# Performance work log

Hardware: AMD Instinct MI355X
Metric: run time of the kernel (lower is better)

## Reference

```python
import jax, jax.numpy as jnp
import numpy as np

N = 50000
E = 1600000
D_IN = 768
NHID = 256
NCLASS = 2


def _spmm(rows, cols, vals, dense):
    # out[i] = sum_{e: rows[e]==i} vals[e] * dense[cols[e]]
    return jax.ops.segment_sum(vals[:, None] * dense[cols], rows, num_segments=N)


def _att_fusion(x1, x2, x3, w):
    # a: [N,3] -> abs -> softmax over the 3 branches
    a = jnp.abs(jnp.concatenate([x1, x2, x3], axis=-1) @ w)
    a = jax.nn.softmax(a, axis=-1)  # [N,3]
    x = jnp.stack([x1, x2, x3], axis=-1)  # [N,H,3]
    return jnp.sum(x * a[:, None, :], axis=-1)  # [N,H]


def setup_inputs() -> dict:
    key = jax.random.key(0)
    ks = jax.random.split(key, 24)

    def u(k, shape, fan):
        s = 1.0 / np.sqrt(fan)
        return jax.random.uniform(k, shape, jnp.float32, -s, s)

    inp = {
        "x": jax.random.normal(ks[0], (N, D_IN), jnp.float32),
        "adj_rows": jax.random.randint(ks[1], (E,), 0, N, jnp.int32),
        "adj_cols": jax.random.randint(ks[2], (E,), 0, N, jnp.int32),
        "adj_vals": jax.random.uniform(ks[3], (E,), jnp.float32),
        "s_rows": jax.random.randint(ks[4], (E,), 0, N, jnp.int32),
        "s_cols": jax.random.randint(ks[5], (E,), 0, N, jnp.int32),
        "s_vals": jax.random.uniform(ks[6], (E,), jnp.float32),
        "W1r1": u(ks[7], (D_IN, NHID), NHID),
        "b1r1": u(ks[8], (NHID,), NHID),
        "W1r2": u(ks[9], (D_IN, NHID), NHID),
        "b1r2": u(ks[10], (NHID,), NHID),
        "mlp1_W": u(ks[11], (D_IN, NHID), D_IN),
        "mlp1_b": u(ks[12], (NHID,), D_IN),
        "af1_w": u(ks[13], (3 * NHID, 3), 3 * NHID),
        "W2r1": u(ks[14], (NHID, NCLASS), NCLASS),
        "b2r1": u(ks[15], (NCLASS,), NCLASS),
        "W2r2": u(ks[16], (NHID, NCLASS), NCLASS),
        "b2r2": u(ks[17], (NCLASS,), NCLASS),
        "mlp2_W": u(ks[18], (NHID, NCLASS), NHID),
        "mlp2_b": u(ks[19], (NCLASS,), NHID),
    }
    return inp


def reference(x, adj_rows, adj_cols, adj_vals, s_rows, s_cols, s_vals,
              W1r1, b1r1, W1r2, b1r2, mlp1_W, mlp1_b, af1_w,
              W2r1, b2r1, W2r2, b2r2, mlp2_W, mlp2_b):
    # dropout in eval mode -> identity
    # layer 1: two sparse GCN branches + tanh MLP branch, attention fused
    x_r1 = _spmm(adj_rows, adj_cols, adj_vals, x @ W1r1) + b1r1
    x_r2 = _spmm(s_rows, s_cols, s_vals, x @ W1r2) + b1r2
    x_1 = jnp.tanh(x @ mlp1_W + mlp1_b)
    x1 = _att_fusion(x_r1, x_r2, x_1, af1_w)  # [N, NHID]

    # layer 2: summed branches
    y_r1 = _spmm(adj_rows, adj_cols, adj_vals, x1 @ W2r1) + b2r1
    y_r2 = _spmm(s_rows, s_cols, s_vals, x1 @ W2r2) + b2r2
    y_1 = jnp.tanh(x1 @ mlp2_W + mlp2_b)
    return y_r2 + y_r1 + y_1  # [N, NCLASS]
```

## Files before the change

kernel.cpp:

```cpp
#include <hip/hip_runtime.h>
#include <hip/hip_bf16.h>

#define NN 50000
#define EE 1600000
#define DIN 768
#define NH 256

typedef unsigned short u16;
typedef unsigned int u32;

typedef __attribute__((ext_vector_type(8))) short short8;
typedef __attribute__((ext_vector_type(4))) float f32x4;

__device__ __forceinline__ float bf2f(u16 u) {
  union { u32 i; float f; } x; x.i = ((u32)u) << 16; return x.f;
}
__device__ __forceinline__ u16 f2bf(float f) {
  union { float f; u32 u; } x; x.f = f;
  u32 r = x.u + 0x7fff + ((x.u >> 16) & 1);
  return (u16)(r >> 16);
}

__global__ __launch_bounds__(256) void prep_kernel(
    const float* __restrict__ X, u16* __restrict__ Xb,
    const int* __restrict__ rA, const int* __restrict__ rB,
    int* __restrict__ cntA, int* __restrict__ cntB,
    const float* __restrict__ Wa, const float* __restrict__ Wb,
    const float* __restrict__ Wc, u16* __restrict__ Wt) {
  int b = blockIdx.x;
  if (b < 37500) {
    size_t idx = (size_t)b * 256 + threadIdx.x;
    float4 v = reinterpret_cast<const float4*>(X)[idx];
    ushort4 o;
    o.x = f2bf(v.x); o.y = f2bf(v.y); o.z = f2bf(v.z); o.w = f2bf(v.w);
    reinterpret_cast<ushort4*>(Xb)[idx] = o;
  } else if (b < 50000) {
    int e = (b - 37500) * 256 + threadIdx.x;
    if (e < EE) atomicAdd(&cntA[rA[e]], 1);
    else        atomicAdd(&cntB[rB[e - EE]], 1);
  } else {
    int idx = (b - 50000) * 256 + threadIdx.x;
    int n = idx / DIN, k = idx - n * DIN;
    const float* W = (n < 256) ? Wa : (n < 512) ? Wb : Wc;
    Wt[idx] = f2bf(W[(size_t)k * NH + (n & 255)]);
  }
}

__global__ __launch_bounds__(256) void scan1(int* __restrict__ cntA, int* __restrict__ rsA,
                                             int* __restrict__ cntB, int* __restrict__ rsB,
                                             int* __restrict__ bsum) {
  int* cnt = (blockIdx.y == 0) ? cntA : cntB;
  int* rs  = (blockIdx.y == 0) ? rsA  : rsB;
  int* bs  = bsum + blockIdx.y * 98;
  __shared__ int wsum[4];
  int t = threadIdx.x, lane = t & 63, wid = t >> 6;
  int i0 = blockIdx.x * 512 + 2 * t;
  int v0 = (i0 < NN) ? cnt[i0] : 0;
  int v1 = (i0 + 1 < NN) ? cnt[i0 + 1] : 0;
  int s = v0 + v1;
  int sc = s;
#pragma unroll
  for (int off = 1; off < 64; off <<= 1) {
    int tv = __shfl_up(sc, off, 64);
    if (lane >= off) sc += tv;
  }
  if (lane == 63) wsum[wid] = sc;
  __syncthreads();
  int woff = 0;
  for (int w = 0; w < wid; ++w) woff += wsum[w];
  int excl = woff + sc - s;
  if (i0 < NN)     { cnt[i0] = excl;          rs[i0 + 1] = excl + v0; }
  if (i0 + 1 < NN) { cnt[i0 + 1] = excl + v0; rs[i0 + 2] = excl + v0 + v1; }
  if (t == 255) bs[blockIdx.x] = woff + sc;
  if (blockIdx.x == 0 && t == 0) rs[0] = 0;
}

__global__ __launch_bounds__(128) void scan2(int* __restrict__ bsum) {
  int* bs = bsum + blockIdx.y * 98;
  __shared__ int tmp[128];
  int t = threadIdx.x;
  int orig = (t < 98) ? bs[t] : 0;
  tmp[t] = orig;
  __syncthreads();
  for (int off = 1; off < 128; off <<= 1) {
    int v = (t >= off) ? tmp[t - off] : 0;
    __syncthreads();
    tmp[t] += v;
    __syncthreads();
  }
  if (t < 98) bs[t] = tmp[t] - orig;
}

__global__ __launch_bounds__(512) void scan3(int* __restrict__ cntA, int* __restrict__ rsA,
                                             int* __restrict__ cntB, int* __restrict__ rsB,
                                             const int* __restrict__ bsum) {
  int* cnt = (blockIdx.y == 0) ? cntA : cntB;
  int* rs  = (blockIdx.y == 0) ? rsA  : rsB;
  int off = bsum[blockIdx.y * 98 + blockIdx.x];
  int i = blockIdx.x * 512 + threadIdx.x;
  if (i < NN) { cnt[i] += off; rs[i + 1] += off; }
}

#define TM 128
#define TN 128
#define TK 32
#define GEMM_BLKS 2346
#define TOT_BLKS (GEMM_BLKS + 12500)

__device__ __forceinline__ void gload16(const u16* g, u16* lds) {
  __builtin_amdgcn_global_load_lds((const __attribute__((address_space(1))) unsigned int*)g,
                                   (__attribute__((address_space(3))) unsigned int*)lds, 16, 0, 0);
}

__global__ __launch_bounds__(256) void gemm_scatter(
    const u16* __restrict__ Xb, const u16* __restrict__ Wt, const float* __restrict__ mlp1_b,
    u16* __restrict__ H1, u16* __restrict__ H2, u16* __restrict__ T,
    const int* __restrict__ rA, const int* __restrict__ cA, const float* __restrict__ vA,
    const int* __restrict__ rB, const int* __restrict__ cB, const float* __restrict__ vB,
    int* __restrict__ curA, u32* __restrict__ edgeA,
    int* __restrict__ curB, u32* __restrict__ edgeB) {
  __shared__ u16 As[TM * TK];
  __shared__ u16 Bs[TN * TK];

  const int b = blockIdx.x;
  const int lo = (b * GEMM_BLKS) / TOT_BLKS;
  const int hi = ((b + 1) * GEMM_BLKS) / TOT_BLKS;

  if (hi > lo) {
    const int gid = lo;
    const int tid = threadIdx.x;
    const int lane = tid & 63;
    const int w = tid >> 6;
    const int n0 = (gid % 6) * TN;
    const int m0 = (gid / 6) * TM;
    const int wm = w >> 1, wn = w & 1;

    f32x4 acc[4][4] = {};

    const int r_l = lane >> 2;
    const int kcp = lane & 3;
    const int r16 = lane & 15;
    const int kcl = lane >> 4;

    for (int k0 = 0; k0 < DIN; k0 += TK) {
#pragma unroll
      for (int q = 0; q < 2; ++q) {
        int row = w * 32 + q * 16 + r_l;
        int kc = kcp ^ ((row >> 1) & 3);
        int gr = m0 + row; if (gr >= NN) gr = NN - 1;
        gload16(Xb + (size_t)gr * DIN + k0 + kc * 8, &As[(w * 32 + q * 16) * TK]);
        gload16(Wt + (size_t)(n0 + row) * DIN + k0 + kc * 8, &Bs[(w * 32 + q * 16) * TK]);
      }
      __syncthreads();

      short8 aF[4], bF[4];
#pragma unroll
      for (int i = 0; i < 4; ++i) {
        int m = wm * 64 + i * 16 + r16;
        aF[i] = *reinterpret_cast<const short8*>(&As[m * TK + (kcl ^ ((m >> 1) & 3)) * 8]);
        int n = wn * 64 + i * 16 + r16;
        bF[i] = *reinterpret_cast<const short8*>(&Bs[n * TK + (kcl ^ ((n >> 1) & 3)) * 8]);
      }
#pragma unroll
      for (int i = 0; i < 4; ++i)
#pragma unroll
        for (int j = 0; j < 4; ++j)
          acc[i][j] = __builtin_amdgcn_mfma_f32_16x16x32_bf16(aF[i], bF[j], acc[i][j], 0, 0, 0);
      __syncthreads();
    }

    const int bsel = n0 >> 8;
    u16* O = (bsel == 0) ? H1 : (bsel == 1) ? H2 : T;
    const int act = (bsel == 2);
    const int cb = n0 & 255;
    const int rq = lane >> 4;
#pragma unroll
    for (int i = 0; i < 4; ++i) {
#pragma unroll
      for (int rr = 0; rr < 4; ++rr) {
        int grow = m0 + wm * 64 + i * 16 + rq * 4 + rr;
        if (grow >= NN) continue;
#pragma unroll
        for (int j = 0; j < 4; ++j) {
          int c = cb + wn * 64 + j * 16 + r16;
          float v = acc[i][j][rr];
          if (act) v = tanhf(v + mlp1_b[c]);
          O[(size_t)grow * NH + c] = f2bf(v);
        }
      }
    }
  } else {
    const int sid = b - lo;
    int e = sid * 256 + threadIdx.x;
    if (e < EE) {
      int r = rA[e];
      int p = atomicAdd(&curA[r], 1);
      edgeA[p] = (u32)(u16)cA[e] | ((u32)f2bf(vA[e]) << 16);
    } else {
      e -= EE;
      int r = rB[e];
      int p = atomicAdd(&curB[r], 1);
      edgeB[p] = (u32)(u16)cB[e] | ((u32)f2bf(vB[e]) << 16);
    }
  }
}

__global__ __launch_bounds__(256) void spmm_fuse(
    const int* __restrict__ rsA, const u32* __restrict__ edgeA,
    const u16* __restrict__ H1, const float* __restrict__ b1,
    const int* __restrict__ rsB, const u32* __restrict__ edgeB,
    const u16* __restrict__ H2, const float* __restrict__ b2,
    const u16* __restrict__ T, const float* __restrict__ afw,
    const float* __restrict__ W2r1, const float* __restrict__ W2r2,
    const float* __restrict__ mlpW, const float* __restrict__ mlpb,
    float* __restrict__ Z1, float* __restrict__ Z2, float* __restrict__ Y1) {
  __shared__ float w[DIN * 3];
  __shared__ float w1[NH * 2], w2[NH * 2], wmm[NH * 2];
  int tid = threadIdx.x;
  for (int i = tid; i < DIN * 3; i += 256) w[i] = afw[i];
  for (int i = tid; i < NH * 2; i += 256) { w1[i] = W2r1[i]; w2[i] = W2r2[i]; wmm[i] = mlpW[i]; }
  __syncthreads();

  int lane = tid & 63, wv = tid >> 6;
  int n = blockIdx.x * 4 + wv;
  int h0 = (lane & 31) * 8;
  int eg = lane >> 5;

  float ac1[8] = {}, ac2[8] = {};
  {
    int s = rsA[n], e = rsA[n + 1];
    int i = s + eg;
    for (; i + 6 < e; i += 8) {
      u32 e0 = edgeA[i], e1 = edgeA[i + 2], e2 = edgeA[i + 4], e3 = edgeA[i + 6];
      short8 v0 = *reinterpret_cast<const short8*>(H1 + (size_t)(e0 & 0xFFFF) * NH + h0);
      short8 v1 = *reinterpret_cast<const short8*>(H1 + (size_t)(e1 & 0xFFFF) * NH + h0);
      short8 v2 = *reinterpret_cast<const short8*>(H1 + (size_t)(e2 & 0xFFFF) * NH + h0);
      short8 v3 = *reinterpret_cast<const short8*>(H1 + (size_t)(e3 & 0xFFFF) * NH + h0);
      float f0 = bf2f((u16)(e0 >> 16)), f1 = bf2f((u16)(e1 >> 16));
      float f2 = bf2f((u16)(e2 >> 16)), f3 = bf2f((u16)(e3 >> 16));
#pragma unroll
      for (int j = 0; j < 8; ++j)
        ac1[j] += f0 * bf2f((u16)v0[j]) + f1 * bf2f((u16)v1[j])
                + f2 * bf2f((u16)v2[j]) + f3 * bf2f((u16)v3[j]);
    }
    for (; i < e; i += 2) {
      u32 e0 = edgeA[i];
      short8 v0 = *reinterpret_cast<const short8*>(H1 + (size_t)(e0 & 0xFFFF) * NH + h0);
      float f0 = bf2f((u16)(e0 >> 16));
#pragma unroll
      for (int j = 0; j < 8; ++j) ac1[j] += f0 * bf2f((u16)v0[j]);
    }
  }
  {
    int s = rsB[n], e = rsB[n + 1];
    int i = s + eg;
    for (; i + 6 < e; i += 8) {
      u32 e0 = edgeB[i], e1 = edgeB[i + 2], e2 = edgeB[i + 4], e3 = edgeB[i + 6];
      short8 v0 = *reinterpret_cast<const short8*>(H2 + (size_t)(e0 & 0xFFFF) * NH + h0);
      short8 v1 = *reinterpret_cast<const short8*>(H2 + (size_t)(e1 & 0xFFFF) * NH + h0);
      short8 v2 = *reinterpret_cast<const short8*>(H2 + (size_t)(e2 & 0xFFFF) * NH + h0);
      short8 v3 = *reinterpret_cast<const short8*>(H2 + (size_t)(e3 & 0xFFFF) * NH + h0);
      float f0 = bf2f((u16)(e0 >> 16)), f1 = bf2f((u16)(e1 >> 16));
      float f2 = bf2f((u16)(e2 >> 16)), f3 = bf2f((u16)(e3 >> 16));
#pragma unroll
      for (int j = 0; j < 8; ++j)
        ac2[j] += f0 * bf2f((u16)v0[j]) + f1 * bf2f((u16)v1[j])
                + f2 * bf2f((u16)v2[j]) + f3 * bf2f((u16)v3[j]);
    }
    for (; i < e; i += 2) {
      u32 e0 = edgeB[i];
      short8 v0 = *reinterpret_cast<const short8*>(H2 + (size_t)(e0 & 0xFFFF) * NH + h0);
      float f0 = bf2f((u16)(e0 >> 16));
#pragma unroll
      for (int j = 0; j < 8; ++j) ac2[j] += f0 * bf2f((u16)v0[j]);
    }
  }
#pragma unroll
  for (int j = 0; j < 8; ++j) {
    ac1[j] += __shfl_xor(ac1[j], 32, 64);
    ac2[j] += __shfl_xor(ac2[j], 32, 64);
  }

  float r1[8], r2[8], t8[8];
  {
    float4 bA0 = *reinterpret_cast<const float4*>(b1 + h0);
    float4 bA1 = *reinterpret_cast<const float4*>(b1 + h0 + 4);
    float4 bB0 = *reinterpret_cast<const float4*>(b2 + h0);
    float4 bB1 = *reinterpret_cast<const float4*>(b2 + h0 + 4);
    float bbA[8] = {bA0.x, bA0.y, bA0.z, bA0.w, bA1.x, bA1.y, bA1.z, bA1.w};
    float bbB[8] = {bB0.x, bB0.y, bB0.z, bB0.w, bB1.x, bB1.y, bB1.z, bB1.w};
    short8 tv = *reinterpret_cast<const short8*>(T + (size_t)n * NH + h0);
#pragma unroll
    for (int j = 0; j < 8; ++j) {
      r1[j] = ac1[j] + bbA[j];
      r2[j] = ac2[j] + bbB[j];
      t8[j] = bf2f((u16)tv[j]);
    }
  }

  float l0 = 0.f, l1 = 0.f, l2 = 0.f;
#pragma unroll
  for (int k = 0; k < 8; ++k) {
    int h = h0 + k;
    l0 += r1[k] * w[h * 3 + 0] + r2[k] * w[(NH + h) * 3 + 0] + t8[k] * w[(2 * NH + h) * 3 + 0];
    l1 += r1[k] * w[h * 3 + 1] + r2[k] * w[(NH + h) * 3 + 1] + t8[k] * w[(2 * NH + h) * 3 + 1];
    l2 += r1[k] * w[h * 3 + 2] + r2[k] * w[(NH + h) * 3 + 2] + t8[k] * w[(2 * NH + h) * 3 + 2];
  }
#pragma unroll
  for (int off = 16; off > 0; off >>= 1) {
    l0 += __shfl_xor(l0, off, 64);
    l1 += __shfl_xor(l1, off, 64);
    l2 += __shfl_xor(l2, off, 64);
  }
  l0 = fabsf(l0); l1 = fabsf(l1); l2 = fabsf(l2);
  float mx = fmaxf(l0, fmaxf(l1, l2));
  float e0 = expf(l0 - mx), e1 = expf(l1 - mx), e2 = expf(l2 - mx);
  float inv = 1.f / (e0 + e1 + e2);
  float s0 = e0 * inv, s1 = e1 * inv, s2 = e2 * inv;

  float p10 = 0.f, p11 = 0.f, p20 = 0.f, p21 = 0.f, p30 = 0.f, p31 = 0.f;
#pragma unroll
  for (int k = 0; k < 8; ++k) {
    int h = h0 + k;
    float xv = s0 * r1[k] + s1 * r2[k] + s2 * t8[k];
    p10 += xv * w1[h * 2 + 0]; p11 += xv * w1[h * 2 + 1];
    p20 += xv * w2[h * 2 + 0]; p21 += xv * w2[h * 2 + 1];
    p30 += xv * wmm[h * 2 + 0]; p31 += xv * wmm[h * 2 + 1];
  }
#pragma unroll
  for (int off = 16; off > 0; off >>= 1) {
    p10 += __shfl_xor(p10, off, 64); p11 += __shfl_xor(p11, off, 64);
    p20 += __shfl_xor(p20, off, 64); p21 += __shfl_xor(p21, off, 64);
    p30 += __shfl_xor(p30, off, 64); p31 += __shfl_xor(p31, off, 64);
  }
  if (lane == 0) {
    Z1[n * 2 + 0] = p10; Z1[n * 2 + 1] = p11;
    Z2[n * 2 + 0] = p20; Z2[n * 2 + 1] = p21;
    Y1[n * 2 + 0] = tanhf(p30 + mlpb[0]);
    Y1[n * 2 + 1] = tanhf(p31 + mlpb[1]);
  }
}

__global__ __launch_bounds__(256) void spmm2_final(
    const int* __restrict__ rsA, const u32* __restrict__ edgeA,
    const int* __restrict__ rsB, const u32* __restrict__ edgeB,
    const float* __restrict__ Z1, const float* __restrict__ Z2, const float* __restrict__ Y1,
    const float* __restrict__ b2r1, const float* __restrict__ b2r2,
    float* __restrict__ out) {
  int tid = threadIdx.x;
  int lane = tid & 63, wave = tid >> 6;
  int n = blockIdx.x * 4 + wave;
  float a0 = 0.f, a1 = 0.f;
  {
    int s = rsA[n], e = rsA[n + 1];
    for (int i = s + lane; i < e; i += 64) {
      u32 ed = edgeA[i];
      float v = bf2f((u16)(ed >> 16));
      float2 z = *reinterpret_cast<const float2*>(Z1 + (ed & 0xFFFF) * 2);
      a0 += v * z.x; a1 += v * z.y;
    }
  }
  float c0 = 0.f, c1 = 0.f;
  {
    int s = rsB[n], e = rsB[n + 1];
    for (int i = s + lane; i < e; i += 64) {
      u32 ed = edgeB[i];
      float v = bf2f((u16)(ed >> 16));
      float2 z = *reinterpret_cast<const float2*>(Z2 + (ed & 0xFFFF) * 2);
      c0 += v * z.x; c1 += v * z.y;
    }
  }
#pragma unroll
  for (int off = 32; off > 0; off >>= 1) {
    a0 += __shfl_down(a0, off, 64); a1 += __shfl_down(a1, off, 64);
    c0 += __shfl_down(c0, off, 64); c1 += __shfl_down(c1, off, 64);
  }
  if (lane == 0) {
    out[n * 2 + 0] = (a0 + b2r1[0]) + (c0 + b2r2[0]) + Y1[n * 2 + 0];
    out[n * 2 + 1] = (a1 + b2r1[1]) + (c1 + b2r2[1]) + Y1[n * 2 + 1];
  }
}

extern "C" void kernel_launch(void* const* d_in, const int* in_sizes, int n_in,
                              void* d_out, int out_size, void* d_ws, size_t ws_size,
                              hipStream_t stream) {
  const float* x        = (const float*)d_in[0];
  const int*   adj_rows = (const int*)d_in[1];
  const int*   adj_cols = (const int*)d_in[2];
  const float* adj_vals = (const float*)d_in[3];
  const int*   s_rows   = (const int*)d_in[4];
  const int*   s_cols   = (const int*)d_in[5];
  const float* s_vals   = (const float*)d_in[6];
  const float* W1r1     = (const float*)d_in[7];
  const float* b1r1     = (const float*)d_in[8];
  const float* W1r2     = (const float*)d_in[9];
  const float* b1r2     = (const float*)d_in[10];
  const float* mlp1_W   = (const float*)d_in[11];
  const float* mlp1_b   = (const float*)d_in[12];
  const float* af1_w    = (const float*)d_in[13];
  const float* W2r1     = (const float*)d_in[14];
  const float* b2r1     = (const float*)d_in[15];
  const float* W2r2     = (const float*)d_in[16];
  const float* b2r2     = (const float*)d_in[17];
  const float* mlp2_W   = (const float*)d_in[18];
  const float* mlp2_b   = (const float*)d_in[19];
  float* out = (float*)d_out;

  char* p = (char*)d_ws;
  auto alloc = [&](size_t b) { char* r = p; p += (b + 255) & ~(size_t)255; return r; };

  char* xb_region = alloc((size_t)NN * DIN * 2);
  u16* Xb = (u16*)xb_region;
  float* Z1 = (float*)xb_region;
  float* Z2 = (float*)(xb_region + (size_t)NN * 2 * 4);
  float* Y1 = (float*)(xb_region + (size_t)NN * 4 * 4);

  u16* H1 = (u16*)alloc((size_t)NN * NH * 2);
  u16* H2 = (u16*)alloc((size_t)NN * NH * 2);
  u16* T  = (u16*)alloc((size_t)NN * NH * 2);
  u16* Wt = (u16*)alloc((size_t)DIN * DIN * 2);
  int* rsA   = (int*)alloc((size_t)(NN + 1) * 4);
  int* curA  = (int*)alloc((size_t)NN * 4);
  u32* edgeA = (u32*)alloc((size_t)EE * 4);
  int* rsB   = (int*)alloc((size_t)(NN + 1) * 4);
  int* curB  = (int*)alloc((size_t)NN * 4);
  u32* edgeB = (u32*)alloc((size_t)EE * 4);
  int* bsum  = (int*)alloc(2 * 98 * 4);

  hipMemsetAsync(curA, 0, (size_t)NN * 4, stream);
  hipMemsetAsync(curB, 0, (size_t)NN * 4, stream);
  prep_kernel<<<52304, 256, 0, stream>>>(x, Xb, adj_rows, s_rows, curA, curB,
                                         W1r1, W1r2, mlp1_W, Wt);

  dim3 gsc(98, 2);
  scan1<<<gsc, 256, 0, stream>>>(curA, rsA, curB, rsB, bsum);
  scan2<<<dim3(1, 2), 128, 0, stream>>>(bsum);
  scan3<<<gsc, 512, 0, stream>>>(curA, rsA, curB, rsB, bsum);

  gemm_scatter<<<TOT_BLKS, 256, 0, stream>>>(Xb, Wt, mlp1_b, H1, H2, T,
                                             adj_rows, adj_cols, adj_vals,
                                             s_rows, s_cols, s_vals,
                                             curA, edgeA, curB, edgeB);

  spmm_fuse<<<NN / 4, 256, 0, stream>>>(rsA, edgeA, H1, b1r1,
                                        rsB, edgeB, H2, b1r2,
                                        T, af1_w, W2r1, W2r2, mlp2_W, mlp2_b,
                                        Z1, Z2, Y1);

  spmm2_final<<<NN / 4, 256, 0, stream>>>(rsA, edgeA, rsB, edgeB,
                                          Z1, Z2, Y1, b2r1, b2r2, out);
}
```

Baseline: 905.6 us.

## Fold scan2 into scan3, batch scatter edges, deepen SpMM unrolling, split final SpMM by half-wave

Drops the separate scan2 launch: each scan3 block now loads the 98 block sums into shared memory and adds up its own prefix. The scatter blocks each handle 4 edges per thread, with row loads, packing and atomics issued in separate batches to expose more memory parallelism. The layer-1 SpMM gains a 16-edge unrolled loop that issues 8 gathers before accumulating. The final SpMM has each half-wave process one adjacency instead of running both sequentially across the full wave. Together these aim to cut launch overhead and raise memory-level parallelism, at the cost of more registers and a changed block balance in the fused GEMM/scatter grid.

```diff
diff --git a/kernel.cpp b/kernel.cpp
--- a/kernel.cpp
+++ b/kernel.cpp
@@ -75,28 +75,16 @@
   if (blockIdx.x == 0 && t == 0) rs[0] = 0;
 }
 
-__global__ __launch_bounds__(128) void scan2(int* __restrict__ bsum) {
-  int* bs = bsum + blockIdx.y * 98;
-  __shared__ int tmp[128];
-  int t = threadIdx.x;
-  int orig = (t < 98) ? bs[t] : 0;
-  tmp[t] = orig;
-  __syncthreads();
-  for (int off = 1; off < 128; off <<= 1) {
-    int v = (t >= off) ? tmp[t - off] : 0;
-    __syncthreads();
-    tmp[t] += v;
-    __syncthreads();
-  }
-  if (t < 98) bs[t] = tmp[t] - orig;
-}
-
 __global__ __launch_bounds__(512) void scan3(int* __restrict__ cntA, int* __restrict__ rsA,
                                              int* __restrict__ cntB, int* __restrict__ rsB,
                                              const int* __restrict__ bsum) {
   int* cnt = (blockIdx.y == 0) ? cntA : cntB;
   int* rs  = (blockIdx.y == 0) ? rsA  : rsB;
-  int off = bsum[blockIdx.y * 98 + blockIdx.x];
+  __shared__ int bs[98];
+  if (threadIdx.x < 98) bs[threadIdx.x] = bsum[blockIdx.y * 98 + threadIdx.x];
+  __syncthreads();
+  int off = 0;
+  for (int k = 0; k < blockIdx.x; ++k) off += bs[k];
   int i = blockIdx.x * 512 + threadIdx.x;
   if (i < NN) { cnt[i] += off; rs[i + 1] += off; }
 }
@@ -105,7 +93,8 @@
 #define TN 128
 #define TK 32
 #define GEMM_BLKS 2346
-#define TOT_BLKS (GEMM_BLKS + 12500)
+#define SCAT_BLKS 3125
+#define TOT_BLKS (GEMM_BLKS + SCAT_BLKS)
 
 __device__ __forceinline__ void gload16(const u16* g, u16* lds) {
   __builtin_amdgcn_global_load_lds((const __attribute__((address_space(1))) unsigned int*)g,
@@ -191,16 +180,24 @@
     }
   } else {
     const int sid = b - lo;
-    int e = sid * 256 + threadIdx.x;
-    if (e < EE) {
-      int r = rA[e];
-      int p = atomicAdd(&curA[r], 1);
-      edgeA[p] = (u32)(u16)cA[e] | ((u32)f2bf(vA[e]) << 16);
-    } else {
-      e -= EE;
-      int r = rB[e];
-      int p = atomicAdd(&curB[r], 1);
-      edgeB[p] = (u32)(u16)cB[e] | ((u32)f2bf(vB[e]) << 16);
+    const int base = sid * 1024 + threadIdx.x;
+    int rws[4]; u32 pks[4];
+#pragma unroll
+    for (int q = 0; q < 4; ++q) {
+      int e = base + q * 256;
+      rws[q] = (e < EE) ? rA[e] : rB[e - EE];
+    }
+#pragma unroll
+    for (int q = 0; q < 4; ++q) {
+      int e = base + q * 256;
+      if (e < EE) pks[q] = (u32)(u16)cA[e] | ((u32)f2bf(vA[e]) << 16);
+      else        pks[q] = (u32)(u16)cB[e - EE] | ((u32)f2bf(vB[e - EE]) << 16);
+    }
+#pragma unroll
+    for (int q = 0; q < 4; ++q) {
+      int e = base + q * 256;
+      if (e < EE) { int p = atomicAdd(&curA[rws[q]], 1); edgeA[p] = pks[q]; }
+      else        { int p = atomicAdd(&curB[rws[q]], 1); edgeB[p] = pks[q]; }
     }
   }
 }
@@ -230,18 +227,35 @@
   {
     int s = rsA[n], e = rsA[n + 1];
     int i = s + eg;
+    for (; i + 14 < e; i += 16) {
+      u32 ew[8];
+#pragma unroll
+      for (int q = 0; q < 8; ++q) ew[q] = edgeA[i + 2 * q];
+      short8 hv[8];
+#pragma unroll
+      for (int q = 0; q < 8; ++q)
+        hv[q] = *reinterpret_cast<const short8*>(H1 + (size_t)(ew[q] & 0xFFFF) * NH + h0);
+#pragma unroll
+      for (int q = 0; q < 8; ++q) {
+        float f = bf2f((u16)(ew[q] >> 16));
+#pragma unroll
+        for (int j = 0; j < 8; ++j) ac1[j] += f * bf2f((u16)hv[q][j]);
+      }
+    }
     for (; i + 6 < e; i += 8) {
-      u32 e0 = edgeA[i], e1 = edgeA[i + 2], e2 = edgeA[i + 4], e3 = edgeA[i + 6];
-      short8 v0 = *reinterpret_cast<const short8*>(H1 + (size_t)(e0 & 0xFFFF) * NH + h0);
-      short8 v1 = *reinterpret_cast<const short8*>(H1 + (size_t)(e1 & 0xFFFF) * NH + h0);
-      short8 v2 = *reinterpret_cast<const short8*>(H1 + (size_t)(e2 & 0xFFFF) * NH + h0);
-      short8 v3 = *reinterpret_cast<const short8*>(H1 + (size_t)(e3 & 0xFFFF) * NH + h0);
-      float f0 = bf2f((u16)(e0 >> 16)), f1 = bf2f((u16)(e1 >> 16));
-      float f2 = bf2f((u16)(e2 >> 16)), f3 = bf2f((u16)(e3 >> 16));
-#pragma unroll
-      for (int j = 0; j < 8; ++j)
-        ac1[j] += f0 * bf2f((u16)v0[j]) + f1 * bf2f((u16)v1[j])
-                + f2 * bf2f((u16)v2[j]) + f3 * bf2f((u16)v3[j]);
+      u32 ew[4];
+#pragma unroll
+      for (int q = 0; q < 4; ++q) ew[q] = edgeA[i + 2 * q];
+      short8 hv[4];
+#pragma unroll
+      for (int q = 0; q < 4; ++q)
+        hv[q] = *reinterpret_cast<const short8*>(H1 + (size_t)(ew[q] & 0xFFFF) * NH + h0);
+#pragma unroll
+      for (int q = 0; q < 4; ++q) {
+        float f = bf2f((u16)(ew[q] >> 16));
+#pragma unroll
+        for (int j = 0; j < 8; ++j) ac1[j] += f * bf2f((u16)hv[q][j]);
+      }
     }
     for (; i < e; i += 2) {
       u32 e0 = edgeA[i];
@@ -254,18 +268,35 @@
   {
     int s = rsB[n], e = rsB[n + 1];
     int i = s + eg;
+    for (; i + 14 < e; i += 16) {
+      u32 ew[8];
+#pragma unroll
+      for (int q = 0; q < 8; ++q) ew[q] = edgeB[i + 2 * q];
+      short8 hv[8];
+#pragma unroll
+      for (int q = 0; q < 8; ++q)
+        hv[q] = *reinterpret_cast<const short8*>(H2 + (size_t)(ew[q] & 0xFFFF) * NH + h0);
+#pragma unroll
+      for (int q = 0; q < 8; ++q) {
+        float f = bf2f((u16)(ew[q] >> 16));
+#pragma unroll
+        for (int j = 0; j < 8; ++j) ac2[j] += f * bf2f((u16)hv[q][j]);
+      }
+    }
     for (; i + 6 < e; i += 8) {
-      u32 e0 = edgeB[i], e1 = edgeB[i + 2], e2 = edgeB[i + 4], e3 = edgeB[i + 6];
-      short8 v0 = *reinterpret_cast<const short8*>(H2 + (size_t)(e0 & 0xFFFF) * NH + h0);
-      short8 v1 = *reinterpret_cast<const short8*>(H2 + (size_t)(e1 & 0xFFFF) * NH + h0);
-      short8 v2 = *reinterpret_cast<const short8*>(H2 + (size_t)(e2 & 0xFFFF) * NH + h0);
-      short8 v3 = *reinterpret_cast<const short8*>(H2 + (size_t)(e3 & 0xFFFF) * NH + h0);
-      float f0 = bf2f((u16)(e0 >> 16)), f1 = bf2f((u16)(e1 >> 16));
-      float f2 = bf2f((u16)(e2 >> 16)), f3 = bf2f((u16)(e3 >> 16));
-#pragma unroll
-      for (int j = 0; j < 8; ++j)
-        ac2[j] += f0 * bf2f((u16)v0[j]) + f1 * bf2f((u16)v1[j])
-                + f2 * bf2f((u16)v2[j]) + f3 * bf2f((u16)v3[j]);
+      u32 ew[4];
+#pragma unroll
+      for (int q = 0; q < 4; ++q) ew[q] = edgeB[i + 2 * q];
+      short8 hv[4];
+#pragma unroll
+      for (int q = 0; q < 4; ++q)
+        hv[q] = *reinterpret_cast<const short8*>(H2 + (size_t)(ew[q] & 0xFFFF) * NH + h0);
+#pragma unroll
+      for (int q = 0; q < 4; ++q) {
+        float f = bf2f((u16)(ew[q] >> 16));
+#pragma unroll
+        for (int j = 0; j < 8; ++j) ac2[j] += f * bf2f((u16)hv[q][j]);
+      }
     }
     for (; i < e; i += 2) {
       u32 e0 = edgeB[i];
@@ -350,34 +381,37 @@
   int tid = threadIdx.x;
   int lane = tid & 63, wave = tid >> 6;
   int n = blockIdx.x * 4 + wave;
+  int half = lane >> 5, l32 = lane & 31;
+  const int* rs = half ? rsB : rsA;
+  const u32* edge = half ? edgeB : edgeA;
+  const float* Z = half ? Z2 : Z1;
   float a0 = 0.f, a1 = 0.f;
-  {
-    int s = rsA[n], e = rsA[n + 1];
-    for (int i = s + lane; i < e; i += 64) {
-      u32 ed = edgeA[i];
-      float v = bf2f((u16)(ed >> 16));
-      float2 z = *reinterpret_cast<const float2*>(Z1 + (ed & 0xFFFF) * 2);
-      a0 += v * z.x; a1 += v * z.y;
-    }
-  }
-  float c0 = 0.f, c1 = 0.f;
-  {
-    int s = rsB[n], e = rsB[n + 1];
-    for (int i = s + lane; i < e; i += 64) {
-      u32 ed = edgeB[i];
-      float v = bf2f((u16)(ed >> 16));
-      float2 z = *reinterpret_cast<const float2*>(Z2 + (ed & 0xFFFF) * 2);
-      c0 += v * z.x; c1 += v * z.y;
-    }
-  }
-#pragma unroll
-  for (int off = 32; off > 0; off >>= 1) {
-    a0 += __shfl_down(a0, off, 64); a1 += __shfl_down(a1, off, 64);
-    c0 += __shfl_down(c0, off, 64); c1 += __shfl_down(c1, off, 64);
-  }
+  int s = rs[n], e = rs[n + 1];
+  int i = s + l32;
+  for (; i + 32 < e; i += 64) {
+    u32 e0 = edge[i], e1 = edge[i + 32];
+    float v0 = bf2f((u16)(e0 >> 16)), v1 = bf2f((u16)(e1 >> 16));
+    float2 z0 = *reinterpret_cast<const float2*>(Z + (e0 & 0xFFFF) * 2);
+    float2 z1 = *reinterpret_cast<const float2*>(Z + (e1 & 0xFFFF) * 2);
+    a0 += v0 * z0.x + v1 * z1.x;
+    a1 += v0 * z0.y + v1 * z1.y;
+  }
+  if (i < e) {
+    u32 e0 = edge[i];
+    float v0 = bf2f((u16)(e0 >> 16));
+    float2 z0 = *reinterpret_cast<const float2*>(Z + (e0 & 0xFFFF) * 2);
+    a0 += v0 * z0.x; a1 += v0 * z0.y;
+  }
+#pragma unroll
+  for (int off = 16; off > 0; off >>= 1) {
+    a0 += __shfl_xor(a0, off, 64);
+    a1 += __shfl_xor(a1, off, 64);
+  }
+  float bsum0 = __shfl(a0, 32, 64);
+  float bsum1 = __shfl(a1, 32, 64);
   if (lane == 0) {
-    out[n * 2 + 0] = (a0 + b2r1[0]) + (c0 + b2r2[0]) + Y1[n * 2 + 0];
-    out[n * 2 + 1] = (a1 + b2r1[1]) + (c1 + b2r2[1]) + Y1[n * 2 + 1];
+    out[n * 2 + 0] = (a0 + b2r1[0]) + (bsum0 + b2r2[0]) + Y1[n * 2 + 0];
+    out[n * 2 + 1] = (a1 + b2r1[1]) + (bsum1 + b2r2[1]) + Y1[n * 2 + 1];
   }
 }
 
@@ -434,8 +468,7 @@
 
   dim3 gsc(98, 2);
   scan1<<<gsc, 256, 0, stream>>>(curA, rsA, curB, rsB, bsum);
-  scan2<<<dim3(1, 2), 128, 0, stream>>>(bsum);
-  scan3<<<gsc, 512, 0, stream>>>(curA, rsA, curB, rsB, bsum);
+  scan3<<<dim3(98, 2), 512, 0, stream>>>(curA, rsA, curB, rsB, bsum);
 
   gemm_scatter<<<TOT_BLKS, 256, 0, stream>>>(Xb, Wt, mlp1_b, H1, H2, T,
                                              adj_rows, adj_cols, adj_vals,
```

Result: faster. 865.2 us (-4.5%).
